# Optimization experiments

Hardware: AMD Instinct MI355X
Metric: run time of the kernel (lower is better)

Reference implementation:

```python
import jax, jax.numpy as jnp
import numpy as np
import math

B, T, D, H, DM = 2, 2048, 1024, 16, 256
DK = D // H

def setup_inputs() -> dict:
    key = jax.random.key(0)
    ks = jax.random.split(key, 13)
    s = 0.02
    return {
        "Hx": jax.random.normal(ks[0], (B, D, T, 1), jnp.float32),
        "Hf": jax.random.normal(ks[1], (B, T, D), jnp.float32),
        "Gm": jax.random.normal(ks[2], (B, T, DM), jnp.float32),
        "Wg": jax.random.normal(ks[3], (T, DM), jnp.float32) * s,
        "bg": jax.random.normal(ks[4], (T,), jnp.float32) * s,
        "Wq": jax.random.normal(ks[5], (D, 2 * D), jnp.float32) * s,
        "bq": jax.random.normal(ks[6], (D,), jnp.float32) * s,
        "Wk": jax.random.normal(ks[7], (D, 2 * D), jnp.float32) * s,
        "bk": jax.random.normal(ks[8], (D,), jnp.float32) * s,
        "Wv": jax.random.normal(ks[9], (D, D), jnp.float32) * s,
        "bv": jax.random.normal(ks[10], (D,), jnp.float32) * s,
        "Wo": jax.random.normal(ks[11], (D, D), jnp.float32) * s,
        "bo": jax.random.normal(ks[12], (D,), jnp.float32) * s,
    }

def reference(Hx, Hf, Gm, Wg, bg, Wq, bq, Wk, bk, Wv, bv, Wo, bo):
    # Hx: (B, D, T, 1) -> (B, T, D)
    hx = jnp.transpose(Hx[..., 0], (0, 2, 1))
    h_cat = jnp.concatenate([hx, Hf], axis=-1)          # (B, T, 2D)
    Q = h_cat @ Wq.T + bq                               # (B, T, D)
    K = h_cat @ Wk.T + bk
    V = hx @ Wv.T + bv
    # split heads: (B, H, T, DK)
    Q = Q.reshape(B, T, H, DK).transpose(0, 2, 1, 3)
    K = K.reshape(B, T, H, DK).transpose(0, 2, 1, 3)
    V = V.reshape(B, T, H, DK).transpose(0, 2, 1, 3)
    scores = jnp.einsum('bhqd,bhkd->bhqk', Q, K) / math.sqrt(DK)
    bias = Gm @ Wg.T + bg                                # (B, T, T)
    scores = scores + bias[:, None, :, :]
    attn = jax.nn.softmax(scores, axis=-1)
    out = jnp.einsum('bhqk,bhkd->bhqd', attn, V)
    out = out.transpose(0, 2, 1, 3).reshape(B, T, D)
    return out @ Wo.T + bo
```

## Files before the change

kernel.cpp:

```cpp
#include <hip/hip_runtime.h>
#include <hip/hip_bf16.h>

using bf16 = __hip_bfloat16;
typedef __attribute__((ext_vector_type(8))) __bf16 bf16x8;
typedef __attribute__((ext_vector_type(4))) float f32x4;

#define GLB_AS(p) ((const __attribute__((address_space(1))) unsigned int*)(p))
#define LDS_AS(p) ((__attribute__((address_space(3))) unsigned int*)(p))

__device__ __forceinline__ void async_copy16(const void* g, void* l) {
  __builtin_amdgcn_global_load_lds(GLB_AS(g), LDS_AS(l), 16, 0, 0);
}

__device__ __forceinline__ f32x4 mfma16x16x32(bf16x8 a, bf16x8 b, f32x4 c) {
  return __builtin_amdgcn_mfma_f32_16x16x32_bf16(a, b, c, 0, 0, 0);
}

__device__ __forceinline__ float bfu2f(unsigned short u) {
  union { unsigned int i; float f; } x;
  x.i = (unsigned int)u << 16;
  return x.f;
}

#define LOG2E 1.44269504f

__global__ __launch_bounds__(256) void pack_hx(const float* __restrict__ Hx,
                                               bf16* __restrict__ hcat) {
  __shared__ float tile[64][65];
  const int t0 = blockIdx.x * 64, d0 = blockIdx.y * 64, b = blockIdx.z;
  const int c = threadIdx.x & 63, r0 = threadIdx.x >> 6;
#pragma unroll
  for (int i = 0; i < 16; ++i) {
    const int rd = r0 + i * 4;
    tile[rd][c] = Hx[((size_t)(b * 1024 + d0 + rd)) * 2048 + t0 + c];
  }
  __syncthreads();
#pragma unroll
  for (int i = 0; i < 16; ++i) {
    const int ct = r0 + i * 4;
    hcat[((size_t)(b * 2048 + t0 + ct)) * 2048 + d0 + c] =
        __float2bfloat16(tile[c][ct]);
  }
}

__global__ __launch_bounds__(256) void pack_all(
    const float* __restrict__ Hf, const float* __restrict__ Wq,
    const float* __restrict__ Wk, const float* __restrict__ Wv,
    const float* __restrict__ Wo, const float* __restrict__ Wg,
    const float* __restrict__ Gm, const float* __restrict__ bq,
    const float* __restrict__ bk, const float* __restrict__ bv,
    bf16* __restrict__ hcat, bf16* __restrict__ Wqkvb, bf16* __restrict__ Wob,
    bf16* __restrict__ Wgb, bf16* __restrict__ Gmb,
    float* __restrict__ qkvbias) {
  const int gid = blockIdx.x * 256 + threadIdx.x;
  const float* src = nullptr;
  bf16* dst = nullptr;
  int lg = 0, ldo = 0, off = 0, idx = 0;
  bool zero = false;
  if (gid < 1048576) { idx = gid; src = Hf; dst = hcat; lg = 8; ldo = 2048; off = 1024; }
  else if (gid < 1572864) { idx = gid - 1048576; src = Wq; dst = Wqkvb; lg = 9; ldo = 2048; }
  else if (gid < 2097152) { idx = gid - 1572864; src = Wk; dst = Wqkvb + (size_t)1024 * 2048; lg = 9; ldo = 2048; }
  else if (gid < 2359296) { idx = gid - 2097152; src = Wv; dst = Wqkvb + (size_t)2048 * 2048; lg = 8; ldo = 2048; }
  else if (gid < 2621440) { idx = gid - 2359296; zero = true; dst = Wqkvb + (size_t)2048 * 2048 + 1024; lg = 8; ldo = 2048; }
  else if (gid < 2883584) { idx = gid - 2621440; src = Wo; dst = Wob; lg = 8; ldo = 1024; }
  else if (gid < 3014656) { idx = gid - 2883584; src = Wg; dst = Wgb; lg = 6; ldo = 256; }
  else if (gid < 3276800) { idx = gid - 3014656; src = Gm; dst = Gmb; lg = 6; ldo = 256; }
  else if (gid < 3277056) { const int i = gid - 3276800; ((float4*)qkvbias)[i] = ((const float4*)bq)[i]; return; }
  else if (gid < 3277312) { const int i = gid - 3277056; ((float4*)(qkvbias + 1024))[i] = ((const float4*)bk)[i]; return; }
  else { const int i = gid - 3277312; ((float4*)(qkvbias + 2048))[i] = ((const float4*)bv)[i]; return; }
  const int row = idx >> lg, c = idx & ((1 << lg) - 1);
  bf16* o = dst + (size_t)row * ldo + off + c * 4;
  __align__(8) bf16 tmp[4];
  if (zero) {
    tmp[0] = tmp[1] = tmp[2] = tmp[3] = __float2bfloat16(0.f);
  } else {
    const float4 v = ((const float4*)src)[(size_t)idx];
    tmp[0] = __float2bfloat16(v.x); tmp[1] = __float2bfloat16(v.y);
    tmp[2] = __float2bfloat16(v.z); tmp[3] = __float2bfloat16(v.w);
  }
  *(ushort4*)o = *(const ushort4*)tmp;
}

__global__ __launch_bounds__(256) void gemm_qkv_bias(
    const bf16* __restrict__ hcat, const bf16* __restrict__ Wqkv,
    const float* __restrict__ qkvbias, const bf16* __restrict__ Gmb,
    const bf16* __restrict__ Wgb, const float* __restrict__ bg,
    bf16* __restrict__ QKb, bf16* __restrict__ Vt, bf16* __restrict__ biasS) {
  __shared__ __align__(16) bf16 As[2][128 * 64];
  __shared__ __align__(16) bf16 Bs[2][128 * 64];
  const int lin = blockIdx.x;
  const int xcd = lin & 7;
  const int kk = lin >> 3;
  const bool isqkv = kk < 96;
  int m_idx, n0;
  if (isqkv) {
    m_idx = kk / 3;
    n0 = (xcd * 3 + (kk - m_idx * 3)) * 128;
  } else {
    const int k2 = kk - 96;
    m_idx = k2 >> 1;
    n0 = (xcd * 2 + (k2 & 1)) * 128;
  }
  const int m0 = m_idx * 128;
  const bf16* A = isqkv ? hcat : Gmb;
  const bf16* W = isqkv ? Wqkv : Wgb;
  const float* biasv = isqkv ? qkvbias : bg;
  const int Kd = isqkv ? 2048 : 256;
  const int tid = threadIdx.x, lane = tid & 63, w = tid >> 6;
  const int wm = (w >> 1) * 64, wn = (w & 1) * 64;
  const int fr = lane & 15;
  const int ck = lane >> 4;

  f32x4 acc[4][4];
  const f32x4 fzero = {0.f, 0.f, 0.f, 0.f};
#pragma unroll
  for (int i = 0; i < 4; ++i)
#pragma unroll
    for (int j = 0; j < 4; ++j) acc[i][j] = fzero;

  auto stage = [&](int it, int buf) {
    const int k0 = it * 64;
#pragma unroll
    for (int is = 0; is < 4; ++is) {
      const int off = is * 4096 + w * 1024;
      const int row = (off >> 7) + (lane >> 3);
      const int sch = ((lane & 7) ^ (row & 7)) * 8;
      async_copy16(A + (size_t)(m0 + row) * Kd + k0 + sch,
                   (char*)As[buf] + off);
      async_copy16(W + (size_t)(n0 + row) * Kd + k0 + sch,
                   (char*)Bs[buf] + off);
    }
  };

  const int nit = Kd >> 6;
  stage(0, 0);
  __syncthreads();
  for (int it = 0; it < nit; ++it) {
    const int cur = it & 1;
    if (it + 1 < nit) stage(it + 1, cur ^ 1);
#pragma unroll
    for (int ks = 0; ks < 2; ++ks) {
      bf16x8 af[4], bfr[4];
#pragma unroll
      for (int i = 0; i < 4; ++i) {
        const int swk = (((ks * 4 + ck) ^ (fr & 7))) * 8;
        af[i] = *(const bf16x8*)(As[cur] + (wm + i * 16 + fr) * 64 + swk);
        bfr[i] = *(const bf16x8*)(Bs[cur] + (wn + i * 16 + fr) * 64 + swk);
      }
#pragma unroll
      for (int i = 0; i < 4; ++i)
#pragma unroll
        for (int j = 0; j < 4; ++j)
          acc[i][j] = mfma16x16x32(af[i], bfr[j], acc[i][j]);
    }
    __syncthreads();
  }
  const int erow = (lane >> 4) * 4;
  const int ecol = lane & 15;

  if (!isqkv) {
#pragma unroll
    for (int i = 0; i < 4; ++i) {
      const int gm0 = m0 + wm + i * 16 + erow;
#pragma unroll
      for (int j = 0; j < 4; ++j) {
        const int gn = n0 + wn + j * 16 + ecol;
        const float bv = biasv[gn];
#pragma unroll
        for (int r = 0; r < 4; ++r)
          biasS[(size_t)(gm0 + r) * 2048 + gn] =
              __float2bfloat16((acc[i][j][r] + bv) * LOG2E);
      }
    }
  } else if (n0 < 2048) {
    const float sc = (n0 < 1024) ? 0.125f * LOG2E : 1.0f;
#pragma unroll
    for (int i = 0; i < 4; ++i) {
      const int gm0 = m0 + wm + i * 16 + erow;
#pragma unroll
      for (int j = 0; j < 4; ++j) {
        const int gn = n0 + wn + j * 16 + ecol;
        const float bv = biasv[gn];
#pragma unroll
        for (int r = 0; r < 4; ++r)
          QKb[(size_t)(gm0 + r) * 2048 + gn] =
              __float2bfloat16((acc[i][j][r] + bv) * sc);
      }
    }
  } else {
#pragma unroll
    for (int i = 0; i < 4; ++i) {
      const int gm0 = m0 + wm + i * 16 + erow;
      const int bb = gm0 >> 11;
      const int t = gm0 & 2047;
#pragma unroll
      for (int j = 0; j < 4; ++j) {
        const int gn = n0 + wn + j * 16 + ecol;
        const float bv = biasv[gn];
        const int d = gn - 2048;
        __align__(8) bf16 tmp[4];
#pragma unroll
        for (int r = 0; r < 4; ++r)
          tmp[r] = __float2bfloat16(acc[i][j][r] + bv);
        *(ushort4*)(Vt + ((size_t)(bb * 1024 + d)) * 2048 + t) =
            *(const ushort4*)tmp;
      }
    }
  }
}

__global__ __launch_bounds__(256) void gemm_out(const bf16* __restrict__ A,
                                                const bf16* __restrict__ W,
                                                const float* __restrict__ biasv,
                                                float* __restrict__ C) {
  __shared__ __align__(16) bf16 As[2][128 * 64];
  __shared__ __align__(16) bf16 Bs[2][64 * 64];
  const int lin = blockIdx.x;
  const int xcd = lin & 7;
  const int kk = lin >> 3;
  const int m0 = (kk >> 1) * 128;
  const int n0 = (xcd * 2 + (kk & 1)) * 64;
  const int tid = threadIdx.x, lane = tid & 63, w = tid >> 6;
  const int wm = (w >> 1) * 64, wn = (w & 1) * 32;
  const int fr = lane & 15;
  const int ck = lane >> 4;

  f32x4 acc[4][2];
  const f32x4 fzero = {0.f, 0.f, 0.f, 0.f};
#pragma unroll
  for (int i = 0; i < 4; ++i)
#pragma unroll
    for (int j = 0; j < 2; ++j) acc[i][j] = fzero;

  auto stage = [&](int it, int buf) {
    const int k0 = it * 64;
#pragma unroll
    for (int is = 0; is < 4; ++is) {
      const int off = is * 4096 + w * 1024;
      const int row = (off >> 7) + (lane >> 3);
      const int sch = ((lane & 7) ^ (row & 7)) * 8;
      async_copy16(A + (size_t)(m0 + row) * 1024 + k0 + sch,
                   (char*)As[buf] + off);
      if (is < 2)
        async_copy16(W + (size_t)(n0 + row) * 1024 + k0 + sch,
                     (char*)Bs[buf] + off);
    }
  };

  stage(0, 0);
  __syncthreads();
  for (int it = 0; it < 16; ++it) {
    const int cur = it & 1;
    if (it + 1 < 16) stage(it + 1, cur ^ 1);
#pragma unroll
    for (int ks = 0; ks < 2; ++ks) {
      bf16x8 af[4], bfr[2];
      const int swk0 = (((ks * 4 + ck) ^ (fr & 7))) * 8;
#pragma unroll
      for (int i = 0; i < 4; ++i)
        af[i] = *(const bf16x8*)(As[cur] + (wm + i * 16 + fr) * 64 + swk0);
#pragma unroll
      for (int j = 0; j < 2; ++j)
        bfr[j] = *(const bf16x8*)(Bs[cur] + (wn + j * 16 + fr) * 64 + swk0);
#pragma unroll
      for (int i = 0; i < 4; ++i)
#pragma unroll
        for (int j = 0; j < 2; ++j)
          acc[i][j] = mfma16x16x32(af[i], bfr[j], acc[i][j]);
    }
    __syncthreads();
  }
  const int erow = (lane >> 4) * 4;
  const int ecol = lane & 15;
#pragma unroll
  for (int i = 0; i < 4; ++i) {
    const int gm0 = m0 + wm + i * 16 + erow;
#pragma unroll
    for (int j = 0; j < 2; ++j) {
      const int gn = n0 + wn + j * 16 + ecol;
      const float bv = biasv[gn];
#pragma unroll
      for (int r = 0; r < 4; ++r)
        C[(size_t)(gm0 + r) * 1024 + gn] = acc[i][j][r] + bv;
    }
  }
}

__global__ __launch_bounds__(256) void flash_attn(
    const bf16* __restrict__ Qm, const bf16* __restrict__ Km,
    const bf16* __restrict__ Vtm, const bf16* __restrict__ biasS,
    float* __restrict__ Op0, float* __restrict__ Op1,
    float* __restrict__ lpart) {
  __shared__ __align__(16) bf16 Ks[2][64 * 64];
  __shared__ __align__(16) bf16 Vs[2][64 * 64];
  __shared__ __align__(16) bf16 Ps[4 * 32 * 72];
  const int lin = blockIdx.x;
  const int xcd = lin & 7;
  const int kk = lin >> 3;
  const int cl = kk & 1;
  const int r2 = kk >> 1;
  const int half = r2 & 1;
  const int q0 = (r2 >> 1) * 128;
  const int combo = xcd * 2 + cl;
  const int hp = combo & 7;
  const int b = combo >> 3;
  const int tid = threadIdx.x, lane = tid & 63, w = tid >> 6;
  const int ql = lane & 15, qk = lane >> 4;
  const int T = 2048, D = 1024;
  const int sw0 = (qk ^ (ql & 7)) * 8;
  const int sw1 = ((qk + 4) ^ (ql & 7)) * 8;

  bf16x8 qf[2][2][2];
#pragma unroll
  for (int hh = 0; hh < 2; ++hh)
#pragma unroll
    for (int qt = 0; qt < 2; ++qt)
#pragma unroll
      for (int ks = 0; ks < 2; ++ks)
        qf[hh][qt][ks] = *(const bf16x8*)(
            Qm + (size_t)(b * T + q0 + w * 32 + qt * 16 + ql) * 2048 +
            (hp * 2 + hh) * 64 + ks * 32 + qk * 8);

  f32x4 acc[2][4][2];
  const f32x4 fzero = {0.f, 0.f, 0.f, 0.f};
#pragma unroll
  for (int hh = 0; hh < 2; ++hh)
#pragma unroll
    for (int dt = 0; dt < 4; ++dt)
#pragma unroll
      for (int qt = 0; qt < 2; ++qt) acc[hh][dt][qt] = fzero;
  float lp[2][2] = {{0.f, 0.f}, {0.f, 0.f}};

  const bf16* kbase0 = Km + (size_t)(b * T) * 2048 + (hp * 2) * 64;
  const bf16* vbase0 = Vtm + (size_t)(b * D + hp * 2 * 64) * 2048;
  const bf16* bb0 = biasS + (size_t)(b * T + q0 + w * 32 + ql) * 2048 + qk * 4;
  bf16* pb = Ps + w * 2304;

  for (int j = 0; j < 16; ++j) {
    const int jj = half * 16 + j;
    __syncthreads();
#pragma unroll
    for (int hh = 0; hh < 2; ++hh)
#pragma unroll
      for (int is = 0; is < 2; ++is) {
        const int off = is * 4096 + w * 1024;
        const int row = (off >> 7) + (lane >> 3);
        const int sch = ((lane & 7) ^ (row & 7)) * 8;
        async_copy16(kbase0 + (size_t)(jj * 64 + row) * 2048 + hh * 64 + sch,
                     (char*)Ks[hh] + off);
        async_copy16(vbase0 + (size_t)(hh * 64 + row) * 2048 + jj * 64 + sch,
                     (char*)Vs[hh] + off);
      }
    ushort4 bq[2][4];
#pragma unroll
    for (int qt = 0; qt < 2; ++qt)
#pragma unroll
      for (int jt = 0; jt < 4; ++jt)
        bq[qt][jt] = *(const ushort4*)(bb0 + (size_t)qt * 16 * 2048 + jj * 64 +
                                       jt * 16);
    __syncthreads();
#pragma unroll
    for (int hh = 0; hh < 2; ++hh) {
      const bf16* ksp = Ks[hh];
      const bf16* vsp = Vs[hh];
#pragma unroll
      for (int jt = 0; jt < 4; ++jt) {
        const bf16x8 kf0 = *(const bf16x8*)(ksp + (jt * 16 + ql) * 64 + sw0);
        const bf16x8 kf1 = *(const bf16x8*)(ksp + (jt * 16 + ql) * 64 + sw1);
#pragma unroll
        for (int qt = 0; qt < 2; ++qt) {
          f32x4 c;
          c[0] = bfu2f(bq[qt][jt].x); c[1] = bfu2f(bq[qt][jt].y);
          c[2] = bfu2f(bq[qt][jt].z); c[3] = bfu2f(bq[qt][jt].w);
          c = mfma16x16x32(kf0, qf[hh][qt][0], c);
          c = mfma16x16x32(kf1, qf[hh][qt][1], c);
          __align__(8) bf16 t4[4];
#pragma unroll
          for (int r = 0; r < 4; ++r) {
            const float pv = __builtin_amdgcn_exp2f(c[r]);
            lp[hh][qt] += pv;
            t4[r] = __float2bfloat16(pv);
          }
          *(ushort4*)(pb + (qt * 16 + ql) * 72 + jt * 16 + qk * 4) =
              *(const ushort4*)t4;
        }
      }
#pragma unroll
      for (int ks = 0; ks < 2; ++ks) {
        const bf16x8 pf0 = *(const bf16x8*)(pb + ql * 72 + ks * 32 + qk * 8);
        const bf16x8 pf1 =
            *(const bf16x8*)(pb + (16 + ql) * 72 + ks * 32 + qk * 8);
        const int sw = ks ? sw1 : sw0;
#pragma unroll
        for (int dt = 0; dt < 4; ++dt) {
          const bf16x8 vf = *(const bf16x8*)(vsp + (dt * 16 + ql) * 64 + sw);
          acc[hh][dt][0] = mfma16x16x32(pf0, vf, acc[hh][dt][0]);
          acc[hh][dt][1] = mfma16x16x32(pf1, vf, acc[hh][dt][1]);
        }
      }
    }
  }
#pragma unroll
  for (int hh = 0; hh < 2; ++hh)
#pragma unroll
    for (int qt = 0; qt < 2; ++qt) {
      lp[hh][qt] += __shfl_xor(lp[hh][qt], 16);
      lp[hh][qt] += __shfl_xor(lp[hh][qt], 32);
    }
  if (qk == 0) {
#pragma unroll
    for (int hh = 0; hh < 2; ++hh)
#pragma unroll
      for (int qt = 0; qt < 2; ++qt)
        lpart[half * 65536 + (b * 16 + hp * 2 + hh) * 2048 + q0 + w * 32 +
              qt * 16 + ql] = lp[hh][qt];
  }
  float* Op = half ? Op1 : Op0;
#pragma unroll
  for (int hh = 0; hh < 2; ++hh)
#pragma unroll
    for (int qt = 0; qt < 2; ++qt)
#pragma unroll
      for (int r = 0; r < 4; ++r) {
        const size_t orow =
            (size_t)(b * T + q0 + w * 32 + qt * 16 + qk * 4 + r);
#pragma unroll
        for (int dt = 0; dt < 4; ++dt)
          Op[orow * 1024 + (hp * 2 + hh) * 64 + dt * 16 + ql] =
              acc[hh][dt][qt][r];
      }
}

__global__ __launch_bounds__(256) void combine(const float* __restrict__ O0,
                                               const float* __restrict__ O1,
                                               const float* __restrict__ lpart,
                                               bf16* __restrict__ AOut) {
  const int idx = blockIdx.x * 256 + threadIdx.x;
  const int row = idx >> 8;
  const int col = (idx & 255) * 4;
  const int b = row >> 11, q = row & 2047, h = col >> 6;
  const int li = (b * 16 + h) * 2048 + q;
  const float inv = __builtin_amdgcn_rcpf(lpart[li] + lpart[65536 + li]);
  const float4 a = *(const float4*)(O0 + (size_t)row * 1024 + col);
  const float4 c = *(const float4*)(O1 + (size_t)row * 1024 + col);
  __align__(8) bf16 t[4] = {
      __float2bfloat16((a.x + c.x) * inv), __float2bfloat16((a.y + c.y) * inv),
      __float2bfloat16((a.z + c.z) * inv), __float2bfloat16((a.w + c.w) * inv)};
  *(ushort4*)(AOut + (size_t)row * 1024 + col) = *(const ushort4*)t;
}

extern "C" void kernel_launch(void* const* d_in, const int* in_sizes, int n_in,
                              void* d_out, int out_size, void* d_ws,
                              size_t ws_size, hipStream_t stream) {
  (void)in_sizes; (void)n_in; (void)out_size; (void)ws_size;
  const float* Hx = (const float*)d_in[0];
  const float* Hf = (const float*)d_in[1];
  const float* Gm = (const float*)d_in[2];
  const float* Wg = (const float*)d_in[3];
  const float* bg = (const float*)d_in[4];
  const float* Wq = (const float*)d_in[5];
  const float* bq = (const float*)d_in[6];
  const float* Wk = (const float*)d_in[7];
  const float* bk = (const float*)d_in[8];
  const float* Wv = (const float*)d_in[9];
  const float* bv = (const float*)d_in[10];
  const float* Wo = (const float*)d_in[11];
  const float* bo = (const float*)d_in[12];
  float* out = (float*)d_out;

  char* p = (char*)d_ws;
  bf16* hcat = (bf16*)p;   p += (size_t)4096 * 2048 * 2;
  bf16* QKb = (bf16*)p;    p += (size_t)4096 * 2048 * 2;
  bf16* Vtb = (bf16*)p;    p += (size_t)4096 * 1024 * 2;
  bf16* biasS = (bf16*)p;  p += (size_t)4096 * 2048 * 2;
  bf16* AOut = (bf16*)p;   p += (size_t)4096 * 1024 * 2;
  bf16* Wqkvb = (bf16*)p;  p += (size_t)3072 * 2048 * 2;
  bf16* Wob = (bf16*)p;    p += (size_t)1024 * 1024 * 2;
  bf16* Wgb = (bf16*)p;    p += (size_t)2048 * 256 * 2;
  bf16* Gmb = (bf16*)p;    p += (size_t)4096 * 256 * 2;
  float* qkvbias = (float*)p; p += (size_t)3072 * 4;
  float* Op1 = (float*)p;  p += (size_t)4096 * 1024 * 4;
  float* lpart = (float*)p; p += (size_t)2 * 65536 * 4;
  float* Op0 = (float*)hcat;

  pack_hx<<<dim3(32, 16, 2), 256, 0, stream>>>(Hx, hcat);
  pack_all<<<dim3(12803), 256, 0, stream>>>(Hf, Wq, Wk, Wv, Wo, Wg, Gm, bq, bk,
                                            bv, hcat, Wqkvb, Wob, Wgb, Gmb,
                                            qkvbias);
  gemm_qkv_bias<<<dim3(1280), 256, 0, stream>>>(hcat, Wqkvb, qkvbias, Gmb,
                                                Wgb, bg, QKb, Vtb, biasS);
  flash_attn<<<dim3(512), 256, 0, stream>>>(QKb, QKb + 1024, Vtb, biasS,
                                            Op0, Op1, lpart);
  combine<<<dim3(4096), 256, 0, stream>>>(Op0, Op1, lpart, AOut);
  gemm_out<<<dim3(512), 256, 0, stream>>>(AOut, Wob, bo, out);
}
```

Before: 292.5 us.

## Split attention key range three ways and store partial outputs in bf16

Splits the flash-attention key dimension into three chunks instead of two, launching 768 blocks rather than 512 to fill more of the GPU's compute units. Partial outputs are written as bf16 instead of fp32, and the combine kernel sums three partials with 16 elements per thread. The aim is better occupancy and less partial-output traffic. In exchange the combine step reads one more buffer, bf16 partials lose precision, and workspace buffers (hcat, Wqkvb) are reused as scratch.

```diff
diff --git a/kernel.cpp b/kernel.cpp
--- a/kernel.cpp
+++ b/kernel.cpp
@@ -289,7 +289,7 @@
 __global__ __launch_bounds__(256) void flash_attn(
     const bf16* __restrict__ Qm, const bf16* __restrict__ Km,
     const bf16* __restrict__ Vtm, const bf16* __restrict__ biasS,
-    float* __restrict__ Op0, float* __restrict__ Op1,
+    bf16* __restrict__ Op0, bf16* __restrict__ Op1, bf16* __restrict__ Op2,
     float* __restrict__ lpart) {
   __shared__ __align__(16) bf16 Ks[2][64 * 64];
   __shared__ __align__(16) bf16 Vs[2][64 * 64];
@@ -299,11 +299,13 @@
   const int kk = lin >> 3;
   const int cl = kk & 1;
   const int r2 = kk >> 1;
-  const int half = r2 & 1;
-  const int q0 = (r2 >> 1) * 128;
+  const int third = r2 % 3;
+  const int q0 = (r2 / 3) * 128;
   const int combo = xcd * 2 + cl;
   const int hp = combo & 7;
   const int b = combo >> 3;
+  const int jstart = third * 11;
+  const int jcount = (third < 2) ? 11 : 10;
   const int tid = threadIdx.x, lane = tid & 63, w = tid >> 6;
   const int ql = lane & 15, qk = lane >> 4;
   const int T = 2048, D = 1024;
@@ -336,8 +338,8 @@
   const bf16* bb0 = biasS + (size_t)(b * T + q0 + w * 32 + ql) * 2048 + qk * 4;
   bf16* pb = Ps + w * 2304;
 
-  for (int j = 0; j < 16; ++j) {
-    const int jj = half * 16 + j;
+  for (int j = 0; j < jcount; ++j) {
+    const int jj = jstart + j;
     __syncthreads();
 #pragma unroll
     for (int hh = 0; hh < 2; ++hh)
@@ -412,10 +414,10 @@
     for (int hh = 0; hh < 2; ++hh)
 #pragma unroll
       for (int qt = 0; qt < 2; ++qt)
-        lpart[half * 65536 + (b * 16 + hp * 2 + hh) * 2048 + q0 + w * 32 +
+        lpart[third * 65536 + (b * 16 + hp * 2 + hh) * 2048 + q0 + w * 32 +
               qt * 16 + ql] = lp[hh][qt];
   }
-  float* Op = half ? Op1 : Op0;
+  bf16* Op = (third == 0) ? Op0 : ((third == 1) ? Op1 : Op2);
 #pragma unroll
   for (int hh = 0; hh < 2; ++hh)
 #pragma unroll
@@ -427,26 +429,37 @@
 #pragma unroll
         for (int dt = 0; dt < 4; ++dt)
           Op[orow * 1024 + (hp * 2 + hh) * 64 + dt * 16 + ql] =
-              acc[hh][dt][qt][r];
-      }
-}
-
-__global__ __launch_bounds__(256) void combine(const float* __restrict__ O0,
-                                               const float* __restrict__ O1,
+              __float2bfloat16(acc[hh][dt][qt][r]);
+      }
+}
+
+__global__ __launch_bounds__(256) void combine(const bf16* __restrict__ O0,
+                                               const bf16* __restrict__ O1,
+                                               const bf16* __restrict__ O2,
                                                const float* __restrict__ lpart,
                                                bf16* __restrict__ AOut) {
   const int idx = blockIdx.x * 256 + threadIdx.x;
-  const int row = idx >> 8;
-  const int col = (idx & 255) * 4;
+  const int row = idx >> 6;
+  const int col = (idx & 63) * 16;
   const int b = row >> 11, q = row & 2047, h = col >> 6;
   const int li = (b * 16 + h) * 2048 + q;
-  const float inv = __builtin_amdgcn_rcpf(lpart[li] + lpart[65536 + li]);
-  const float4 a = *(const float4*)(O0 + (size_t)row * 1024 + col);
-  const float4 c = *(const float4*)(O1 + (size_t)row * 1024 + col);
-  __align__(8) bf16 t[4] = {
-      __float2bfloat16((a.x + c.x) * inv), __float2bfloat16((a.y + c.y) * inv),
-      __float2bfloat16((a.z + c.z) * inv), __float2bfloat16((a.w + c.w) * inv)};
-  *(ushort4*)(AOut + (size_t)row * 1024 + col) = *(const ushort4*)t;
+  const float inv = __builtin_amdgcn_rcpf(lpart[li] + lpart[65536 + li] +
+                                          lpart[131072 + li]);
+  const size_t base = (size_t)row * 1024 + col;
+  const ushort4* a4 = (const ushort4*)(O0 + base);
+  const ushort4* c4 = (const ushort4*)(O1 + base);
+  const ushort4* d4 = (const ushort4*)(O2 + base);
+  ushort4* o4 = (ushort4*)(AOut + base);
+#pragma unroll
+  for (int g = 0; g < 4; ++g) {
+    const ushort4 a = a4[g], c = c4[g], d = d4[g];
+    __align__(8) bf16 t[4] = {
+        __float2bfloat16((bfu2f(a.x) + bfu2f(c.x) + bfu2f(d.x)) * inv),
+        __float2bfloat16((bfu2f(a.y) + bfu2f(c.y) + bfu2f(d.y)) * inv),
+        __float2bfloat16((bfu2f(a.z) + bfu2f(c.z) + bfu2f(d.z)) * inv),
+        __float2bfloat16((bfu2f(a.w) + bfu2f(c.w) + bfu2f(d.w)) * inv)};
+    o4[g] = *(const ushort4*)t;
+  }
 }
 
 extern "C" void kernel_launch(void* const* d_in, const int* in_sizes, int n_in,
@@ -479,9 +492,10 @@
   bf16* Wgb = (bf16*)p;    p += (size_t)2048 * 256 * 2;
   bf16* Gmb = (bf16*)p;    p += (size_t)4096 * 256 * 2;
   float* qkvbias = (float*)p; p += (size_t)3072 * 4;
-  float* Op1 = (float*)p;  p += (size_t)4096 * 1024 * 4;
-  float* lpart = (float*)p; p += (size_t)2 * 65536 * 4;
-  float* Op0 = (float*)hcat;
+  bf16* Op1 = (bf16*)p;    p += (size_t)4096 * 1024 * 2;
+  float* lpart = (float*)p; p += (size_t)3 * 65536 * 4;
+  bf16* Op0 = hcat;
+  bf16* Op2 = Wqkvb;
 
   pack_hx<<<dim3(32, 16, 2), 256, 0, stream>>>(Hx, hcat);
   pack_all<<<dim3(12803), 256, 0, stream>>>(Hf, Wq, Wk, Wv, Wo, Wg, Gm, bq, bk,
@@ -489,8 +503,8 @@
                                             qkvbias);
   gemm_qkv_bias<<<dim3(1280), 256, 0, stream>>>(hcat, Wqkvb, qkvbias, Gmb,
                                                 Wgb, bg, QKb, Vtb, biasS);
-  flash_attn<<<dim3(512), 256, 0, stream>>>(QKb, QKb + 1024, Vtb, biasS,
-                                            Op0, Op1, lpart);
-  combine<<<dim3(4096), 256, 0, stream>>>(Op0, Op1, lpart, AOut);
+  flash_attn<<<dim3(768), 256, 0, stream>>>(QKb, QKb + 1024, Vtb, biasS,
+                                            Op0, Op1, Op2, lpart);
+  combine<<<dim3(1024), 256, 0, stream>>>(Op0, Op1, Op2, lpart, AOut);
   gemm_out<<<dim3(512), 256, 0, stream>>>(AOut, Wob, bo, out);
 }
```

New measurement: 331.8 us. 1.13x slower.
